# Kernel tuning notes

Measured on AMD Instinct MI355X. Metric: run time of the kernel, lower is better.

Reference implementation:

```python
import jax, jax.numpy as jnp
import numpy as np

B, H, L, D = 2, 16, 2048, 64


def setup_inputs() -> dict:
    key = jax.random.key(0)
    kq, kk, kv = jax.random.split(key, 3)
    queries = jax.random.normal(kq, (B, H, L, D), dtype=jnp.float32)
    keys = jax.random.normal(kk, (B, H, L, D), dtype=jnp.float32)
    values = jax.random.normal(kv, (B, H, L, D), dtype=jnp.float32)
    # causal mask: True = masked (as consumed by masked_fill in the original)
    attn_mask = jnp.triu(jnp.ones((L, L), dtype=bool), k=1)
    return {"queries": queries, "keys": keys, "values": values, "attn_mask": attn_mask}


def reference(queries, keys, values, attn_mask):
    D_ = queries.shape[-1]
    scale = 1.0 / jnp.sqrt(jnp.asarray(D_, dtype=queries.dtype))
    # [B,H,Lq,Lk] score matrix (faithfully materialized as in the original)
    scores = jnp.einsum("bhqd,bhkd->bhqk", queries, keys) * scale
    scores = jnp.where(attn_mask, jnp.asarray(-1e9, dtype=scores.dtype), scores)
    attention = jax.nn.softmax(scores, axis=-1)
    # dropout rate = 0.0 (inference); identity
    out = jnp.einsum("bhqk,bhkd->bhqd", attention, values)
    return out
```

## Files before the change

kernel.cpp:

```cpp
#include <hip/hip_runtime.h>


constexpr int Lq = 2048;
constexpr int Dh = 64;
constexpr int TILEB = 16384;
constexpr int VOFF  = 8192;

typedef __attribute__((ext_vector_type(16))) float f32x16;
typedef __attribute__((ext_vector_type(4))) float f32x4;
typedef __attribute__((ext_vector_type(8))) unsigned short u16x8;
typedef __attribute__((ext_vector_type(4))) unsigned int u32x4;
typedef __attribute__((ext_vector_type(8))) __bf16 bf16x8;

__device__ __forceinline__ unsigned short f2bf(float f) {
  __bf16 h = (__bf16)f;
  return __builtin_bit_cast(unsigned short, h);
}
__device__ __forceinline__ unsigned cvtpk(float lo, float hi) {
  unsigned r;
  asm("v_cvt_pk_bf16_f32 %0, %1, %2" : "=v"(r) : "v"(lo), "v"(hi));
  return r;
}
__device__ __forceinline__ f32x16 mfma32(u16x8 a, u16x8 b, f32x16 c) {
  return __builtin_amdgcn_mfma_f32_32x32x16_bf16(
      __builtin_bit_cast(bf16x8, a), __builtin_bit_cast(bf16x8, b), c, 0, 0, 0);
}
__device__ __forceinline__ void plswap(unsigned a, unsigned b,
                                       unsigned& wlo, unsigned& whi) {
#if __has_builtin(__builtin_amdgcn_permlane32_swap)
  auto r = __builtin_amdgcn_permlane32_swap((int)a, (int)b, false, false);
  wlo = (unsigned)r[0];
  whi = (unsigned)r[1];
#else
  const int hh = (threadIdx.x >> 5) & 1;
  unsigned pa = (unsigned)__shfl_xor((int)a, 32);
  unsigned pb = (unsigned)__shfl_xor((int)b, 32);
  wlo = hh ? pb : a;
  whi = hh ? b : pa;
#endif
}

__global__ __launch_bounds__(256, 2)
void repack(const float* __restrict__ K, const float* __restrict__ V,
            unsigned char* __restrict__ W) {
  __shared__ unsigned short Vl[64][72];

  const int tid = threadIdx.x;
  const int bt  = blockIdx.x;
  const int bh  = bt >> 5;
  const int tl  = bt & 31;
  const size_t src = (size_t)bh * Lq * Dh + (size_t)tl * 64 * Dh;
  unsigned char* img = W + (size_t)bt * TILEB;

  const int r  = tid >> 2;
  const int c2 = (tid & 3) * 2;

  {
    const float* kp = K + src + (size_t)r * Dh + c2 * 8;
    f32x4 a = *(const f32x4*)kp;
    f32x4 b = *(const f32x4*)(kp + 4);
    f32x4 c = *(const f32x4*)(kp + 8);
    f32x4 d = *(const f32x4*)(kp + 12);
    u16x8 lo, hi;
    #pragma unroll
    for (int j = 0; j < 4; ++j) {
      lo[j] = f2bf(a[j]); lo[4 + j] = f2bf(b[j]);
      hi[j] = f2bf(c[j]); hi[4 + j] = f2bf(d[j]);
    }
    *(u16x8*)(img + (c2 * 64 + r) * 16)       = lo;
    *(u16x8*)(img + ((c2 + 1) * 64 + r) * 16) = hi;
  }
  {
    const float* vp = V + src + (size_t)r * Dh + c2 * 8;
    f32x4 a = *(const f32x4*)vp;
    f32x4 b = *(const f32x4*)(vp + 4);
    f32x4 c = *(const f32x4*)(vp + 8);
    f32x4 d = *(const f32x4*)(vp + 12);
    u16x8 lo, hi;
    #pragma unroll
    for (int j = 0; j < 4; ++j) {
      lo[j] = f2bf(a[j]); lo[4 + j] = f2bf(b[j]);
      hi[j] = f2bf(c[j]); hi[4 + j] = f2bf(d[j]);
    }
    *(u16x8*)&Vl[r][c2 * 8]     = lo;
    *(u16x8*)&Vl[r][c2 * 8 + 8] = hi;
  }
  __syncthreads();
  {
    u16x8 lo, hi;
    #pragma unroll
    for (int e = 0; e < 8; ++e) {
      lo[e] = Vl[c2 * 8 + e][r];
      hi[e] = Vl[c2 * 8 + 8 + e][r];
    }
    *(u16x8*)(img + VOFF + (c2 * 64 + r) * 16)       = lo;
    *(u16x8*)(img + VOFF + ((c2 + 1) * 64 + r) * 16) = hi;
  }
}

__global__ __launch_bounds__(256, 2)
void fattn_fwd(const float* __restrict__ Q, const unsigned char* __restrict__ W,
               float* __restrict__ O) {
  __shared__ float Mrg[3][64][33];

  const int tid  = threadIdx.x;
  const int lane = tid & 63;
  const int w    = tid >> 6;
  const int l31  = lane & 31;
  const int h    = lane >> 5;

  const int bid = blockIdx.x;
  const int xcd = bid & 7;
  const int s_  = bid >> 3;
  const int bh  = xcd * 4 + (s_ & 3);
  const int qg  = 63 - (s_ >> 2);
  const int qmin = qg * 32;
  const size_t base = (size_t)bh * Lq * Dh;

  u16x8 qc[4];
  {
    const float* qp = Q + base + (size_t)(qmin + l31) * Dh + h * 8;
    #pragma unroll
    for (int dc = 0; dc < 4; ++dc) {
      f32x4 lo = *(const f32x4*)(qp + dc * 16);
      f32x4 hi = *(const f32x4*)(qp + dc * 16 + 4);
      u16x8 f;
      #pragma unroll
      for (int j = 0; j < 4; ++j) { f[j] = f2bf(lo[j]); f[4 + j] = f2bf(hi[j]); }
      qc[dc] = f;
    }
  }

  const int Sw = qg + 1 - w;
  const int nw = (Sw > 0) ? ((Sw + 3) >> 2) : 0;

  const unsigned char* Wb = W + (size_t)(bh * 32) * TILEB;
  const int laneK = ((w & 1) * 32 + l31) * 16 + h * 1024;
  const int laneV = VOFF + ((w & 1) * 4 + h) * 1024 + l31 * 16;

  f32x16 accO0, accO1;
  #pragma unroll
  for (int i = 0; i < 16; ++i) { accO0[i] = 0.f; accO1[i] = 0.f; }
  float ls0 = 0.f, ls1 = 0.f, ls2 = 0.f, ls3 = 0.f;

  const float C1 = 0.125f * 1.4426950408889634f;
  const float C0 = -10.0f * 1.4426950408889634f;

  auto ldK = [&](u16x8 (&kf)[4], const unsigned char* pT) {
    const unsigned char* p = pT + laneK;
    kf[0] = *(const u16x8*)(p);
    kf[1] = *(const u16x8*)(p + 2048);
    kf[2] = *(const u16x8*)(p + 4096);
    kf[3] = *(const u16x8*)(p + 6144);
  };
  auto ldV = [&](u16x8 (&vf)[4], const unsigned char* pT) {
    const unsigned char* p = pT + laneV;
    vf[0] = *(const u16x8*)(p);
    vf[1] = *(const u16x8*)(p + 512);
    vf[2] = *(const u16x8*)(p + 2048);
    vf[3] = *(const u16x8*)(p + 2560);
  };

  auto qk = [&](const u16x8 (&kf)[4]) -> f32x16 {
    f32x16 s;
    #pragma unroll
    for (int i = 0; i < 16; ++i) s[i] = 0.f;
    __builtin_amdgcn_s_setprio(1);
    #pragma unroll
    for (int dc = 0; dc < 4; ++dc) s = mfma32(kf[dc], qc[dc], s);
    __builtin_amdgcn_s_setprio(0);
    return s;
  };

  auto spv = [&](const f32x16& s, const u16x8 (&vf)[4], int kv0) {
    float p[16];
    if (kv0 + 31 > qmin) {
      const int qrow = qmin + l31;
      #pragma unroll
      for (int r = 0; r < 16; ++r) {
        float e = __builtin_amdgcn_exp2f(s[r] * C1 + C0);
        const int kvg = kv0 + (r & 3) + 8 * (r >> 2) + 4 * h;
        p[r] = (kvg <= qrow) ? e : 0.0f;
      }
    } else {
      #pragma unroll
      for (int r = 0; r < 16; ++r)
        p[r] = __builtin_amdgcn_exp2f(s[r] * C1 + C0);
    }
    ls0 += (p[0] + p[1]) + (p[2] + p[3]);
    ls1 += (p[4] + p[5]) + (p[6] + p[7]);
    ls2 += (p[8] + p[9]) + (p[10] + p[11]);
    ls3 += (p[12] + p[13]) + (p[14] + p[15]);

    unsigned pk[4][2];
    #pragma unroll
    for (int q4 = 0; q4 < 4; ++q4) {
      pk[q4][0] = cvtpk(p[q4 * 4 + 0], p[q4 * 4 + 1]);
      pk[q4][1] = cvtpk(p[q4 * 4 + 2], p[q4 * 4 + 3]);
    }
    __builtin_amdgcn_s_setprio(1);
    #pragma unroll
    for (int c2 = 0; c2 < 2; ++c2) {
      unsigned w0, w1, w2, w3;
      plswap(pk[2 * c2][0], pk[2 * c2 + 1][0], w0, w2);
      plswap(pk[2 * c2][1], pk[2 * c2 + 1][1], w1, w3);
      u32x4 pw = {w0, w1, w2, w3};
      u16x8 pf = __builtin_bit_cast(u16x8, pw);
      accO0 = mfma32(vf[c2 * 2 + 0], pf, accO0);
      accO1 = mfma32(vf[c2 * 2 + 1], pf, accO1);
    }
    __builtin_amdgcn_s_setprio(0);
  };

  if (nw > 0) {
    const unsigned char* pT = Wb + (size_t)(w >> 1) * TILEB;
    u16x8 kA[4], kB[4], vA[4], vB[4];
    ldK(kA, pT);
    ldV(vA, pT);
    int j = 0;
    int kv0 = w * 32;
    while (j + 2 <= nw) {
      ldK(kB, pT + 2 * TILEB);
      ldV(vB, pT + 2 * TILEB);
      __builtin_amdgcn_sched_barrier(0);
      {
        f32x16 s = qk(kA);
        spv(s, vA, kv0);
      }
      if (j + 2 < nw) {
        ldK(kA, pT + 4 * TILEB);
        ldV(vA, pT + 4 * TILEB);
      }
      __builtin_amdgcn_sched_barrier(0);
      {
        f32x16 s = qk(kB);
        spv(s, vB, kv0 + 128);
      }
      j += 2; pT += 4 * TILEB; kv0 += 256;
    }
    if (j < nw) {
      f32x16 s = qk(kA);
      spv(s, vA, kv0);
    }
  }

  const float lsum = (ls0 + ls1) + (ls2 + ls3);
  __syncthreads();
  if (w != 0) {
    float* m = &Mrg[w - 1][lane][0];
    #pragma unroll
    for (int r = 0; r < 16; ++r) { m[r] = accO0[r]; m[16 + r] = accO1[r]; }
    m[32] = lsum;
  }
  __syncthreads();
  if (w == 0) {
    float a0[16], a1[16];
    float ls = lsum;
    #pragma unroll
    for (int r = 0; r < 16; ++r) { a0[r] = accO0[r]; a1[r] = accO1[r]; }
    #pragma unroll
    for (int v = 0; v < 3; ++v) {
      const float* m = &Mrg[v][lane][0];
      #pragma unroll
      for (int r = 0; r < 16; ++r) { a0[r] += m[r]; a1[r] += m[16 + r]; }
      ls += m[32];
    }
    ls += __shfl_xor(ls, 32);
    const float inv = 1.0f / ls;
    float* op = O + base + (size_t)(qmin + l31) * Dh;
    #pragma unroll
    for (int r = 0; r < 16; ++r) {
      const int d = (r & 3) + 8 * (r >> 2) + 4 * h;
      op[d]      = a0[r] * inv;
      op[32 + d] = a1[r] * inv;
    }
  }
}

extern "C" void kernel_launch(void* const* d_in, const int* in_sizes, int n_in,
                              void* d_out, int out_size, void* d_ws, size_t ws_size,
                              hipStream_t stream) {
  const float* Q = (const float*)d_in[0];
  const float* K = (const float*)d_in[1];
  const float* V = (const float*)d_in[2];
  float* O = (float*)d_out;
  unsigned char* W = (unsigned char*)d_ws;

  repack<<<dim3(1024), dim3(256), 0, stream>>>(K, V, W);
  fattn_fwd<<<dim3(2048), dim3(256), 0, stream>>>(Q, W, O);
}
```

Baseline: 48.42 us.

## Drop register double-buffering, raise occupancy, and remap blocks for causal balance

Removes the manually double-buffered K/V register prefetch and puts the loads inline in a simple per-tile loop, which cuts register pressure. Launch bounds rise from 2 to 4 blocks per CU so more waves can hide memory latency. The block-to-(head, query-group) mapping is changed to interleave query groups in a serpentine order, spreading heavy and light causal rows more evenly across XCDs and launch time. The trade-off is losing explicit load/compute overlap inside each wave, which now depends on having more waves resident.

```diff
diff --git a/kernel.cpp b/kernel.cpp
--- a/kernel.cpp
+++ b/kernel.cpp
@@ -98,7 +98,7 @@
   }
 }
 
-__global__ __launch_bounds__(256, 2)
+__global__ __launch_bounds__(256, 4)
 void fattn_fwd(const float* __restrict__ Q, const unsigned char* __restrict__ W,
                float* __restrict__ O) {
   __shared__ float Mrg[3][64][33];
@@ -110,10 +110,10 @@
   const int h    = lane >> 5;
 
   const int bid = blockIdx.x;
-  const int xcd = bid & 7;
-  const int s_  = bid >> 3;
-  const int bh  = xcd * 4 + (s_ & 3);
-  const int qg  = 63 - (s_ >> 2);
+  const int bh  = (bid & 7) * 4 + ((bid >> 3) & 3);
+  const int v_  = (bid >> 5) & 7;
+  const int m_  = bid >> 8;
+  const int qg  = 8 * (7 - m_) + ((m_ & 1) ? v_ : (7 - v_));
   const int qmin = qg * 32;
   const size_t base = (size_t)bh * Lq * Dh;
 
@@ -146,101 +146,74 @@
   const float C1 = 0.125f * 1.4426950408889634f;
   const float C0 = -10.0f * 1.4426950408889634f;
 
-  auto ldK = [&](u16x8 (&kf)[4], const unsigned char* pT) {
-    const unsigned char* p = pT + laneK;
-    kf[0] = *(const u16x8*)(p);
-    kf[1] = *(const u16x8*)(p + 2048);
-    kf[2] = *(const u16x8*)(p + 4096);
-    kf[3] = *(const u16x8*)(p + 6144);
-  };
-  auto ldV = [&](u16x8 (&vf)[4], const unsigned char* pT) {
-    const unsigned char* p = pT + laneV;
-    vf[0] = *(const u16x8*)(p);
-    vf[1] = *(const u16x8*)(p + 512);
-    vf[2] = *(const u16x8*)(p + 2048);
-    vf[3] = *(const u16x8*)(p + 2560);
-  };
-
-  auto qk = [&](const u16x8 (&kf)[4]) -> f32x16 {
-    f32x16 s;
-    #pragma unroll
-    for (int i = 0; i < 16; ++i) s[i] = 0.f;
-    __builtin_amdgcn_s_setprio(1);
-    #pragma unroll
-    for (int dc = 0; dc < 4; ++dc) s = mfma32(kf[dc], qc[dc], s);
-    __builtin_amdgcn_s_setprio(0);
-    return s;
-  };
-
-  auto spv = [&](const f32x16& s, const u16x8 (&vf)[4], int kv0) {
-    float p[16];
-    if (kv0 + 31 > qmin) {
-      const int qrow = qmin + l31;
-      #pragma unroll
-      for (int r = 0; r < 16; ++r) {
-        float e = __builtin_amdgcn_exp2f(s[r] * C1 + C0);
-        const int kvg = kv0 + (r & 3) + 8 * (r >> 2) + 4 * h;
-        p[r] = (kvg <= qrow) ? e : 0.0f;
-      }
-    } else {
-      #pragma unroll
-      for (int r = 0; r < 16; ++r)
-        p[r] = __builtin_amdgcn_exp2f(s[r] * C1 + C0);
-    }
-    ls0 += (p[0] + p[1]) + (p[2] + p[3]);
-    ls1 += (p[4] + p[5]) + (p[6] + p[7]);
-    ls2 += (p[8] + p[9]) + (p[10] + p[11]);
-    ls3 += (p[12] + p[13]) + (p[14] + p[15]);
-
-    unsigned pk[4][2];
-    #pragma unroll
-    for (int q4 = 0; q4 < 4; ++q4) {
-      pk[q4][0] = cvtpk(p[q4 * 4 + 0], p[q4 * 4 + 1]);
-      pk[q4][1] = cvtpk(p[q4 * 4 + 2], p[q4 * 4 + 3]);
-    }
-    __builtin_amdgcn_s_setprio(1);
-    #pragma unroll
-    for (int c2 = 0; c2 < 2; ++c2) {
-      unsigned w0, w1, w2, w3;
-      plswap(pk[2 * c2][0], pk[2 * c2 + 1][0], w0, w2);
-      plswap(pk[2 * c2][1], pk[2 * c2 + 1][1], w1, w3);
-      u32x4 pw = {w0, w1, w2, w3};
-      u16x8 pf = __builtin_bit_cast(u16x8, pw);
-      accO0 = mfma32(vf[c2 * 2 + 0], pf, accO0);
-      accO1 = mfma32(vf[c2 * 2 + 1], pf, accO1);
-    }
-    __builtin_amdgcn_s_setprio(0);
-  };
-
   if (nw > 0) {
     const unsigned char* pT = Wb + (size_t)(w >> 1) * TILEB;
-    u16x8 kA[4], kB[4], vA[4], vB[4];
-    ldK(kA, pT);
-    ldV(vA, pT);
-    int j = 0;
     int kv0 = w * 32;
-    while (j + 2 <= nw) {
-      ldK(kB, pT + 2 * TILEB);
-      ldV(vB, pT + 2 * TILEB);
-      __builtin_amdgcn_sched_barrier(0);
+    for (int j = 0; j < nw; ++j) {
+      u16x8 kf[4], vf[4];
       {
-        f32x16 s = qk(kA);
-        spv(s, vA, kv0);
-      }
-      if (j + 2 < nw) {
-        ldK(kA, pT + 4 * TILEB);
-        ldV(vA, pT + 4 * TILEB);
-      }
-      __builtin_amdgcn_sched_barrier(0);
+        const unsigned char* p = pT + laneK;
+        kf[0] = *(const u16x8*)(p);
+        kf[1] = *(const u16x8*)(p + 2048);
+        kf[2] = *(const u16x8*)(p + 4096);
+        kf[3] = *(const u16x8*)(p + 6144);
+      }
       {
-        f32x16 s = qk(kB);
-        spv(s, vB, kv0 + 128);
-      }
-      j += 2; pT += 4 * TILEB; kv0 += 256;
-    }
-    if (j < nw) {
-      f32x16 s = qk(kA);
-      spv(s, vA, kv0);
+        const unsigned char* p = pT + laneV;
+        vf[0] = *(const u16x8*)(p);
+        vf[1] = *(const u16x8*)(p + 512);
+        vf[2] = *(const u16x8*)(p + 2048);
+        vf[3] = *(const u16x8*)(p + 2560);
+      }
+
+      f32x16 s;
+      #pragma unroll
+      for (int i = 0; i < 16; ++i) s[i] = 0.f;
+      __builtin_amdgcn_s_setprio(1);
+      #pragma unroll
+      for (int dc = 0; dc < 4; ++dc) s = mfma32(kf[dc], qc[dc], s);
+      __builtin_amdgcn_s_setprio(0);
+
+      float p[16];
+      if (kv0 + 31 > qmin) {
+        const int qrow = qmin + l31;
+        #pragma unroll
+        for (int r = 0; r < 16; ++r) {
+          float e = __builtin_amdgcn_exp2f(s[r] * C1 + C0);
+          const int kvg = kv0 + (r & 3) + 8 * (r >> 2) + 4 * h;
+          p[r] = (kvg <= qrow) ? e : 0.0f;
+        }
+      } else {
+        #pragma unroll
+        for (int r = 0; r < 16; ++r)
+          p[r] = __builtin_amdgcn_exp2f(s[r] * C1 + C0);
+      }
+      ls0 += (p[0] + p[1]) + (p[2] + p[3]);
+      ls1 += (p[4] + p[5]) + (p[6] + p[7]);
+      ls2 += (p[8] + p[9]) + (p[10] + p[11]);
+      ls3 += (p[12] + p[13]) + (p[14] + p[15]);
+
+      unsigned pk[4][2];
+      #pragma unroll
+      for (int q4 = 0; q4 < 4; ++q4) {
+        pk[q4][0] = cvtpk(p[q4 * 4 + 0], p[q4 * 4 + 1]);
+        pk[q4][1] = cvtpk(p[q4 * 4 + 2], p[q4 * 4 + 3]);
+      }
+      __builtin_amdgcn_s_setprio(1);
+      #pragma unroll
+      for (int c2 = 0; c2 < 2; ++c2) {
+        unsigned w0, w1, w2, w3;
+        plswap(pk[2 * c2][0], pk[2 * c2 + 1][0], w0, w2);
+        plswap(pk[2 * c2][1], pk[2 * c2 + 1][1], w1, w3);
+        u32x4 pw = {w0, w1, w2, w3};
+        u16x8 pf = __builtin_bit_cast(u16x8, pw);
+        accO0 = mfma32(vf[c2 * 2 + 0], pf, accO0);
+        accO1 = mfma32(vf[c2 * 2 + 1], pf, accO1);
+      }
+      __builtin_amdgcn_s_setprio(0);
+
+      pT += 2 * TILEB;
+      kv0 += 128;
     }
   }
 
@@ -259,8 +232,8 @@
     #pragma unroll
     for (int r = 0; r < 16; ++r) { a0[r] = accO0[r]; a1[r] = accO1[r]; }
     #pragma unroll
-    for (int v = 0; v < 3; ++v) {
-      const float* m = &Mrg[v][lane][0];
+    for (int vv = 0; vv < 3; ++vv) {
+      const float* m = &Mrg[vv][lane][0];
       #pragma unroll
       for (int r = 0; r < 16; ++r) { a0[r] += m[r]; a1[r] += m[16 + r]; }
       ls += m[32];
```

Measured after the change: 47.01 us. 2.9% less time.
